# Optimization experiments

Measured on AMD Instinct MI355X. Metric: run time of the kernel, lower is better.

Reference implementation:

```python
import jax, jax.numpy as jnp
import numpy as np

N, D = 65536, 256

def setup_inputs() -> dict:
    key = jax.random.key(0)
    k1, k2, k3 = jax.random.split(key, 3)
    x = jax.random.normal(k1, (N, D), dtype=jnp.float32)
    x_fit = jax.random.normal(k2, (N, D), dtype=jnp.float32)
    # S_inv buffer: a symmetric PD-ish matrix (eye at init; use random SPD for generality)
    A = jax.random.normal(k3, (D, D), dtype=jnp.float32) / np.sqrt(D)
    S_inv = A @ A.T + jnp.eye(D, dtype=jnp.float32)
    return {"x": x, "x_fit": x_fit, "S_inv": S_inv}

def reference(x, x_fit, S_inv):
    # diag(delta @ S_inv @ delta.T) computed row-wise without the NxN intermediate
    delta = x - x_fit                     # [N, D]
    t = delta @ S_inv                     # [N, D]
    return jnp.sum(t * delta, axis=-1)    # [N]
```

## Files before the change

kernel.cpp:

```cpp
#include <hip/hip_runtime.h>
#include <hip/hip_bf16.h>
#include <stdint.h>


#define D 256
#define BLOCK_T 512
#define ROWS_PER_TILE 64
#define NT 4
#define LDS_STRIDE 272

typedef __attribute__((ext_vector_type(4))) float f32x4;
typedef __attribute__((ext_vector_type(8))) short bf16x8;
typedef __attribute__((ext_vector_type(4))) short bf16x4;

static __device__ __forceinline__ unsigned short f2bf(float f) {
    union { float f; uint32_t u; } v; v.f = f;
    uint32_t u = v.u;
    return (unsigned short)((u + 0x7FFFu + ((u >> 16) & 1u)) >> 16);
}
static __device__ __forceinline__ float bf2f(unsigned short s) {
    union { uint32_t u; float f; } v; v.u = ((uint32_t)s) << 16;
    return v.f;
}

static __device__ __forceinline__ f32x4 gload4f(const float* p) {
    f32x4 r;
    asm volatile("global_load_dwordx4 %0, %1, off" : "=v"(r) : "v"(p));
    return r;
}

__global__ void prep_S_kernel(const float* __restrict__ S, unsigned short* __restrict__ Sb) {
    int i = (blockIdx.x * 256 + threadIdx.x) * 4;
    f32x4 v = *(const f32x4*)(S + i);
    uint32_t lo = (uint32_t)f2bf(v[0]) | ((uint32_t)f2bf(v[1]) << 16);
    uint32_t hi = (uint32_t)f2bf(v[2]) | ((uint32_t)f2bf(v[3]) << 16);
    *(uint2*)(Sb + i) = make_uint2(lo, hi);
}

__global__ __launch_bounds__(BLOCK_T, 2) void mahal_kernel(
    const float* __restrict__ x, const float* __restrict__ xf,
    const unsigned short* __restrict__ Sb, float* __restrict__ out)
{
    __shared__ unsigned short ld[ROWS_PER_TILE * LDS_STRIDE];
    __shared__ float psum[8 * ROWS_PER_TILE];

    const int t    = threadIdx.x;
    const int w    = t >> 6;
    const int lane = t & 63;
    const int lo4  = lane & 15;
    const int hi2  = lane >> 4;
    const int lrow0 = t >> 5;
    const int col   = (t & 31) * 8;
    const int blockRow0 = blockIdx.x * (NT * ROWS_PER_TILE);

    bf16x8 b0[8], b1[8];
    {
        const unsigned short* Sp = Sb + (w * 32 + lo4) * D + hi2 * 8;
        #pragma unroll
        for (int kb = 0; kb < 8; ++kb) {
            b0[kb] = *(const bf16x8*)(Sp + kb * 32);
            b1[kb] = *(const bf16x8*)(Sp + 16 * D + kb * 32);
        }
    }

    f32x4 xa[4], xb[4], fa[4], fb[4];
    #pragma unroll
    for (int i = 0; i < 4; ++i) {
        const int g = (blockRow0 + i * 16 + lrow0) * D + col;
        xa[i] = gload4f(x + g);
        xb[i] = gload4f(x + g + 4);
        fa[i] = gload4f(xf + g);
        fb[i] = gload4f(xf + g + 4);
    }

    for (int j = 0; j < NT; ++j) {
        asm volatile("s_waitcnt vmcnt(0)" ::: "memory");
        __builtin_amdgcn_sched_barrier(0);

        if (j > 0) {
            asm volatile("s_waitcnt lgkmcnt(0)" ::: "memory");
            __builtin_amdgcn_s_barrier();
            if (t < ROWS_PER_TILE) {
                float s = 0.f;
                #pragma unroll
                for (int ww = 0; ww < 8; ++ww) s += psum[ww * ROWS_PER_TILE + t];
                out[blockRow0 + (j - 1) * ROWS_PER_TILE + t] = s;
            }
        }

        #pragma unroll
        for (int i = 0; i < 4; ++i) {
            bf16x8 o;
            o[0] = (short)f2bf(xa[i][0] - fa[i][0]);
            o[1] = (short)f2bf(xa[i][1] - fa[i][1]);
            o[2] = (short)f2bf(xa[i][2] - fa[i][2]);
            o[3] = (short)f2bf(xa[i][3] - fa[i][3]);
            o[4] = (short)f2bf(xb[i][0] - fb[i][0]);
            o[5] = (short)f2bf(xb[i][1] - fb[i][1]);
            o[6] = (short)f2bf(xb[i][2] - fb[i][2]);
            o[7] = (short)f2bf(xb[i][3] - fb[i][3]);
            *(bf16x8*)(&ld[(i * 16 + lrow0) * LDS_STRIDE + col]) = o;
        }

        if (j + 1 < NT) {
            #pragma unroll
            for (int i = 0; i < 4; ++i) {
                const int g = (blockRow0 + (j + 1) * ROWS_PER_TILE + i * 16 + lrow0) * D + col;
                xa[i] = gload4f(x + g);
                xb[i] = gload4f(x + g + 4);
                fa[i] = gload4f(xf + g);
                fb[i] = gload4f(xf + g + 4);
            }
        }

        asm volatile("s_waitcnt lgkmcnt(0)" ::: "memory");
        __builtin_amdgcn_s_barrier();
        __builtin_amdgcn_sched_barrier(0);

        #pragma unroll
        for (int rt = 0; rt < 4; ++rt) {
            f32x4 acc0 = (f32x4){0.f, 0.f, 0.f, 0.f};
            f32x4 acc1 = (f32x4){0.f, 0.f, 0.f, 0.f};
            const unsigned short* A = &ld[(rt * 16 + lo4) * LDS_STRIDE + hi2 * 8];
            #pragma unroll
            for (int kb = 0; kb < 8; ++kb) {
                bf16x8 a = *(const bf16x8*)(A + kb * 32);
                acc0 = __builtin_amdgcn_mfma_f32_16x16x32_bf16(b0[kb], a, acc0, 0, 0, 0);
                acc1 = __builtin_amdgcn_mfma_f32_16x16x32_bf16(b1[kb], a, acc1, 0, 0, 0);
            }
            const unsigned short* dr = &ld[(rt * 16 + lo4) * LDS_STRIDE + w * 32 + hi2 * 4];
            bf16x4 d0 = *(const bf16x4*)(dr);
            bf16x4 d1 = *(const bf16x4*)(dr + 16);
            float pr = 0.f;
            #pragma unroll
            for (int r = 0; r < 4; ++r) {
                pr += acc0[r] * bf2f((unsigned short)d0[r]);
                pr += acc1[r] * bf2f((unsigned short)d1[r]);
            }
            pr += __shfl_xor(pr, 16, 64);
            pr += __shfl_xor(pr, 32, 64);
            if (lane < 16)
                psum[w * ROWS_PER_TILE + rt * 16 + lane] = pr;
        }
    }

    asm volatile("s_waitcnt lgkmcnt(0)" ::: "memory");
    __builtin_amdgcn_s_barrier();
    if (t < ROWS_PER_TILE) {
        float s = 0.f;
        #pragma unroll
        for (int ww = 0; ww < 8; ++ww) s += psum[ww * ROWS_PER_TILE + t];
        out[blockRow0 + (NT - 1) * ROWS_PER_TILE + t] = s;
    }
}

extern "C" void kernel_launch(void* const* d_in, const int* in_sizes, int n_in,
                              void* d_out, int out_size, void* d_ws, size_t ws_size,
                              hipStream_t stream) {
    const float* x  = (const float*)d_in[0];
    const float* xf = (const float*)d_in[1];
    const float* S  = (const float*)d_in[2];
    float* out = (float*)d_out;
    unsigned short* Sb = (unsigned short*)d_ws;

    prep_S_kernel<<<(D * D) / (256 * 4), 256, 0, stream>>>(S, Sb);

    const int nRows = in_sizes[0] / D;
    const int nBlocks = nRows / (NT * ROWS_PER_TILE);
    mahal_kernel<<<nBlocks, BLOCK_T, 0, stream>>>(x, xf, Sb, out);
}
```

Before: 35.92 us.

## Fuse S_inv bf16 conversion into main kernel and halve row tile for occupancy

Drops the separate prep kernel that converted S_inv to bf16. Each block now loads the fp32 matrix directly and converts its B fragments in registers, which removes one launch and the workspace round trip. The row tile shrinks from 64 to 32 rows, doubling the grid, and launch bounds now request 4 blocks per CU. In exchange every block reads twice as many bytes of S (fp32 instead of bf16), and many more blocks redo the same conversion.

```diff
diff --git a/kernel.cpp b/kernel.cpp
--- a/kernel.cpp
+++ b/kernel.cpp
@@ -5,7 +5,7 @@
 
 #define D 256
 #define BLOCK_T 512
-#define ROWS_PER_TILE 64
+#define ROWS_PER_TILE 32
 #define NT 4
 #define LDS_STRIDE 272
 
@@ -22,6 +22,14 @@
     union { uint32_t u; float f; } v; v.u = ((uint32_t)s) << 16;
     return v.f;
 }
+static __device__ __forceinline__ bf16x8 cvt8(f32x4 lo, f32x4 hi) {
+    bf16x8 o;
+    o[0] = (short)f2bf(lo[0]); o[1] = (short)f2bf(lo[1]);
+    o[2] = (short)f2bf(lo[2]); o[3] = (short)f2bf(lo[3]);
+    o[4] = (short)f2bf(hi[0]); o[5] = (short)f2bf(hi[1]);
+    o[6] = (short)f2bf(hi[2]); o[7] = (short)f2bf(hi[3]);
+    return o;
+}
 
 static __device__ __forceinline__ f32x4 gload4f(const float* p) {
     f32x4 r;
@@ -29,17 +37,9 @@
     return r;
 }
 
-__global__ void prep_S_kernel(const float* __restrict__ S, unsigned short* __restrict__ Sb) {
-    int i = (blockIdx.x * 256 + threadIdx.x) * 4;
-    f32x4 v = *(const f32x4*)(S + i);
-    uint32_t lo = (uint32_t)f2bf(v[0]) | ((uint32_t)f2bf(v[1]) << 16);
-    uint32_t hi = (uint32_t)f2bf(v[2]) | ((uint32_t)f2bf(v[3]) << 16);
-    *(uint2*)(Sb + i) = make_uint2(lo, hi);
-}
-
-__global__ __launch_bounds__(BLOCK_T, 2) void mahal_kernel(
+__global__ __launch_bounds__(BLOCK_T, 4) void mahal_kernel(
     const float* __restrict__ x, const float* __restrict__ xf,
-    const unsigned short* __restrict__ Sb, float* __restrict__ out)
+    const float* __restrict__ S, float* __restrict__ out)
 {
     __shared__ unsigned short ld[ROWS_PER_TILE * LDS_STRIDE];
     __shared__ float psum[8 * ROWS_PER_TILE];
@@ -48,24 +48,28 @@
     const int w    = t >> 6;
     const int lane = t & 63;
     const int lo4  = lane & 15;
-    const int hi2  = lane >> 4;
+    const int kg   = lane >> 4;
     const int lrow0 = t >> 5;
     const int col   = (t & 31) * 8;
     const int blockRow0 = blockIdx.x * (NT * ROWS_PER_TILE);
 
     bf16x8 b0[8], b1[8];
     {
-        const unsigned short* Sp = Sb + (w * 32 + lo4) * D + hi2 * 8;
+        const float* Sp = S + (w * 32 + lo4) * D + kg * 8;
         #pragma unroll
         for (int kb = 0; kb < 8; ++kb) {
-            b0[kb] = *(const bf16x8*)(Sp + kb * 32);
-            b1[kb] = *(const bf16x8*)(Sp + 16 * D + kb * 32);
+            f32x4 l0 = *(const f32x4*)(Sp + kb * 32);
+            f32x4 h0 = *(const f32x4*)(Sp + kb * 32 + 4);
+            b0[kb] = cvt8(l0, h0);
+            f32x4 l1 = *(const f32x4*)(Sp + 16 * D + kb * 32);
+            f32x4 h1 = *(const f32x4*)(Sp + 16 * D + kb * 32 + 4);
+            b1[kb] = cvt8(l1, h1);
         }
     }
 
-    f32x4 xa[4], xb[4], fa[4], fb[4];
+    f32x4 xa[2], xb[2], fa[2], fb[2];
     #pragma unroll
-    for (int i = 0; i < 4; ++i) {
+    for (int i = 0; i < 2; ++i) {
         const int g = (blockRow0 + i * 16 + lrow0) * D + col;
         xa[i] = gload4f(x + g);
         xb[i] = gload4f(x + g + 4);
@@ -89,7 +93,7 @@
         }
 
         #pragma unroll
-        for (int i = 0; i < 4; ++i) {
+        for (int i = 0; i < 2; ++i) {
             bf16x8 o;
             o[0] = (short)f2bf(xa[i][0] - fa[i][0]);
             o[1] = (short)f2bf(xa[i][1] - fa[i][1]);
@@ -104,7 +108,7 @@
 
         if (j + 1 < NT) {
             #pragma unroll
-            for (int i = 0; i < 4; ++i) {
+            for (int i = 0; i < 2; ++i) {
                 const int g = (blockRow0 + (j + 1) * ROWS_PER_TILE + i * 16 + lrow0) * D + col;
                 xa[i] = gload4f(x + g);
                 xb[i] = gload4f(x + g + 4);
@@ -118,17 +122,17 @@
         __builtin_amdgcn_sched_barrier(0);
 
         #pragma unroll
-        for (int rt = 0; rt < 4; ++rt) {
+        for (int rt = 0; rt < 2; ++rt) {
             f32x4 acc0 = (f32x4){0.f, 0.f, 0.f, 0.f};
             f32x4 acc1 = (f32x4){0.f, 0.f, 0.f, 0.f};
-            const unsigned short* A = &ld[(rt * 16 + lo4) * LDS_STRIDE + hi2 * 8];
+            const unsigned short* A = &ld[(rt * 16 + lo4) * LDS_STRIDE + kg * 8];
             #pragma unroll
             for (int kb = 0; kb < 8; ++kb) {
                 bf16x8 a = *(const bf16x8*)(A + kb * 32);
                 acc0 = __builtin_amdgcn_mfma_f32_16x16x32_bf16(b0[kb], a, acc0, 0, 0, 0);
                 acc1 = __builtin_amdgcn_mfma_f32_16x16x32_bf16(b1[kb], a, acc1, 0, 0, 0);
             }
-            const unsigned short* dr = &ld[(rt * 16 + lo4) * LDS_STRIDE + w * 32 + hi2 * 4];
+            const unsigned short* dr = &ld[(rt * 16 + lo4) * LDS_STRIDE + w * 32 + kg * 4];
             bf16x4 d0 = *(const bf16x4*)(dr);
             bf16x4 d1 = *(const bf16x4*)(dr + 16);
             float pr = 0.f;
@@ -161,11 +165,8 @@
     const float* xf = (const float*)d_in[1];
     const float* S  = (const float*)d_in[2];
     float* out = (float*)d_out;
-    unsigned short* Sb = (unsigned short*)d_ws;
-
-    prep_S_kernel<<<(D * D) / (256 * 4), 256, 0, stream>>>(S, Sb);
 
     const int nRows = in_sizes[0] / D;
     const int nBlocks = nRows / (NT * ROWS_PER_TILE);
-    mahal_kernel<<<nBlocks, BLOCK_T, 0, stream>>>(x, xf, Sb, out);
+    mahal_kernel<<<nBlocks, BLOCK_T, 0, stream>>>(x, xf, S, out);
 }
```

New measurement: 62.65 us. 74.4% more time.
